# Kernel tuning notes

Measured on AMD Instinct MI355X. Metric: run time of the kernel, lower is better.

## Reference

```python
import jax, jax.numpy as jnp
import numpy as np

EPS = 1e-7  # K.epsilon()

def squash(v, axis=-1):
    sn = jnp.sum(jnp.square(v), axis=axis, keepdims=True)
    scale = sn / (1.0 + sn) / jnp.sqrt(sn + EPS)
    return scale * v

def setup_inputs() -> dict:
    key = jax.random.key(0)
    k1, k2, k3 = jax.random.split(key, 3)
    B, In, Din = 32, 2048, 8
    N, Dout, C = 64, 16, 32
    x = jax.random.normal(k1, (B, In, Din), dtype=jnp.float32)
    W = jax.random.normal(k2, (N, C, Dout, Din), dtype=jnp.float32) * 0.1
    B_bias = jax.random.normal(k3, (N, Dout), dtype=jnp.float32) * 0.1
    return {"x": x, "W": W, "B_bias": B_bias}

def reference(x, W, B_bias):
    routings = 3
    N, C, Dout, Din = W.shape
    In = x.shape[1]
    # repeat channel weights to cover all input capsules: [N, In, Dout, Din]
    W2 = jnp.repeat(W, In // C, axis=1)
    # vote vectors: inputs_hat[b,n,i,d] = sum_k x[b,i,k] * W2[n,i,d,k]
    inputs_hat = jnp.einsum('bik,nidk->bnid', x, W2)  # [B, N, In, Dout]
    b = jnp.zeros(inputs_hat.shape[:3], dtype=inputs_hat.dtype)  # [B, N, In]
    outputs = None
    for i in range(routings):
        c = jax.nn.softmax(b, axis=1)  # softmax over num_capsule axis
        s = jnp.einsum('bni,bnid->bnd', c, inputs_hat) + B_bias
        outputs = squash(s)
        if i < routings - 1:
            b = b + jnp.einsum('bnd,bnid->bni', outputs, inputs_hat)
    return outputs
```

## Files before the change

kernel.cpp:

```cpp
#include <hip/hip_runtime.h>
#include <math.h>

constexpr int B_    = 32;
constexpr int In_   = 2048;
constexpr int Din_  = 8;
constexpr int N_    = 64;
constexpr int Dout_ = 16;
constexpr int C_    = 32;
constexpr int ICP   = 64;
constexpr float EPS = 1e-7f;


__global__ __launch_bounds__(256) void caps_v0(
    const float* __restrict__ x, const float* __restrict__ W,
    const float* __restrict__ bias, float* __restrict__ v0)
{
    const int b = blockIdx.x >> 3, j = blockIdx.x & 7;
    const int t = threadIdx.x;

    __shared__ float xbar[C_][Din_];

    {
        const int c = t >> 3, k = t & 7;
        const float* xp = x + (size_t)b * In_ * Din_ + (size_t)c * ICP * Din_ + k;
        float acc = 0.f;
        #pragma unroll 8
        for (int i = 0; i < ICP; ++i) acc += xp[i * Din_];
        xbar[c][k] = acc * (1.f / 64.f);
    }
    __syncthreads();

    {
        const int nl = t >> 5, lane32 = t & 31;
        const int d = lane32 >> 1, h = lane32 & 1;
        const int n = j * 8 + nl;

        float a = 0.f;
        #pragma unroll
        for (int cc = 0; cc < 16; ++cc) {
            const int c2 = cc * 2 + h;
            const float4* wp = (const float4*)(W + (((size_t)n * C_ + c2) * Dout_ + d) * Din_);
            const float4 w0 = wp[0], w1 = wp[1];
            a += w0.x * xbar[c2][0] + w0.y * xbar[c2][1] + w0.z * xbar[c2][2] + w0.w * xbar[c2][3]
               + w1.x * xbar[c2][4] + w1.y * xbar[c2][5] + w1.z * xbar[c2][6] + w1.w * xbar[c2][7];
        }
        a += __shfl_xor(a, 1);
        a += bias[n * Dout_ + d];

        float sn = a * a;
        sn += __shfl_xor(sn, 2);
        sn += __shfl_xor(sn, 4);
        sn += __shfl_xor(sn, 8);
        sn += __shfl_xor(sn, 16);
        const float sc = sn / (1.f + sn) / sqrtf(sn + EPS);
        if (h == 0) v0[(size_t)b * 1024 + n * Dout_ + d] = a * sc;
    }
}

__global__ __launch_bounds__(256) void caps_route(
    const float* __restrict__ x, const float* __restrict__ W,
    const float* __restrict__ bias, const float* __restrict__ v0buf,
    const float* __restrict__ s_prev, float* __restrict__ s_next)
{
    const int b = blockIdx.x >> 5;
    const int c = blockIdx.x & 31;
    const int t = threadIdx.x;
    const int w = t >> 6, l = t & 63;
    const int n4 = t >> 2, q4 = t & 3;

    __shared__ float Us[N_][8];
    __shared__ float xs[ICP][8];
    __shared__ float lg[ICP][68];
    __shared__ float ps[4][ICP];
    __shared__ float inv_s[ICP];
    __shared__ float ys[4][N_][8];

    float4 vv;
    {
        const size_t vo = (size_t)b * 1024 + n4 * 16 + q4 * 4;
        const float4 v0v = *(const float4*)(v0buf + vo);
        if (s_prev) {
            float4 a = *(const float4*)(s_prev + vo);
            const float4 bb = *(const float4*)(bias + n4 * 16 + q4 * 4);
            a.x += bb.x; a.y += bb.y; a.z += bb.z; a.w += bb.w;
            float sn = a.x * a.x + a.y * a.y + a.z * a.z + a.w * a.w;
            sn += __shfl_xor(sn, 1);
            sn += __shfl_xor(sn, 2);
            const float sc = sn / (1.f + sn) / sqrtf(sn + EPS);
            vv.x = a.x * sc + v0v.x; vv.y = a.y * sc + v0v.y;
            vv.z = a.z * sc + v0v.z; vv.w = a.w * sc + v0v.w;
        } else {
            vv = v0v;
        }
    }

    {
        const float vd[4] = {vv.x, vv.y, vv.z, vv.w};
        float pU[8] = {0, 0, 0, 0, 0, 0, 0, 0};
        #pragma unroll
        for (int dd = 0; dd < 4; ++dd) {
            const int d = q4 * 4 + dd;
            const float4* wp = (const float4*)(W + (((size_t)n4 * 32 + c) * 16 + d) * 8);
            const float4 w0 = wp[0], w1 = wp[1];
            const float v_ = vd[dd];
            pU[0] += v_ * w0.x; pU[1] += v_ * w0.y; pU[2] += v_ * w0.z; pU[3] += v_ * w0.w;
            pU[4] += v_ * w1.x; pU[5] += v_ * w1.y; pU[6] += v_ * w1.z; pU[7] += v_ * w1.w;
        }
        #pragma unroll
        for (int k = 0; k < 8; ++k) {
            pU[k] += __shfl_xor(pU[k], 1);
            pU[k] += __shfl_xor(pU[k], 2);
        }
        float2 u2; u2.x = pU[2 * q4]; u2.y = pU[2 * q4 + 1];
        *(float2*)&Us[n4][2 * q4] = u2;
    }

    float xr[8];
    {
        const float4* xp = (const float4*)(x + ((size_t)b * In_ + c * ICP + l) * 8);
        const float4 x0 = xp[0], x1 = xp[1];
        xr[0] = x0.x; xr[1] = x0.y; xr[2] = x0.z; xr[3] = x0.w;
        xr[4] = x1.x; xr[5] = x1.y; xr[6] = x1.z; xr[7] = x1.w;
        if (w == 0) { *(float4*)&xs[l][0] = x0; *(float4*)&xs[l][4] = x1; }
    }
    __syncthreads();

    {
        float e[16];
        float ssum = 0.f;
        #pragma unroll
        for (int nn = 0; nn < 16; ++nn) {
            const int n = w * 16 + nn;
            const float4 u0 = *(const float4*)&Us[n][0];
            const float4 u1 = *(const float4*)&Us[n][4];
            const float a = u0.x * xr[0] + u0.y * xr[1] + u0.z * xr[2] + u0.w * xr[3]
                          + u1.x * xr[4] + u1.y * xr[5] + u1.z * xr[6] + u1.w * xr[7];
            const float ee = __expf(a);
            e[nn] = ee; ssum += ee;
        }
        #pragma unroll
        for (int qq = 0; qq < 4; ++qq) {
            float4 o;
            o.x = e[qq * 4 + 0]; o.y = e[qq * 4 + 1]; o.z = e[qq * 4 + 2]; o.w = e[qq * 4 + 3];
            *(float4*)&lg[l][w * 16 + qq * 4] = o;
        }
        ps[w][l] = ssum;
    }
    __syncthreads();

    if (t < 64) inv_s[t] = 1.f / (ps[0][t] + ps[1][t] + ps[2][t] + ps[3][t]);
    __syncthreads();

    {
        const int nq = l >> 2, kq = l & 3;
        float y[8] = {0, 0, 0, 0, 0, 0, 0, 0};
        #pragma unroll
        for (int ii = 0; ii < 16; ++ii) {
            const int i = w * 16 + ii;
            const float4 cw = *(const float4*)&lg[i][nq * 4];
            const float iv = inv_s[i];
            const float2 x2 = *(const float2*)&xs[i][kq * 2];
            const float c0 = cw.x * iv, c1 = cw.y * iv, c2 = cw.z * iv, c3 = cw.w * iv;
            y[0] += c0 * x2.x; y[1] += c0 * x2.y;
            y[2] += c1 * x2.x; y[3] += c1 * x2.y;
            y[4] += c2 * x2.x; y[5] += c2 * x2.y;
            y[6] += c3 * x2.x; y[7] += c3 * x2.y;
        }
        #pragma unroll
        for (int jj = 0; jj < 4; ++jj) {
            float2 o; o.x = y[2 * jj]; o.y = y[2 * jj + 1];
            *(float2*)&ys[w][nq * 4 + jj][kq * 2] = o;
        }
    }
    __syncthreads();

    {
        float yn[8];
        #pragma unroll
        for (int k = 0; k < 8; ++k)
            yn[k] = ys[0][n4][k] + ys[1][n4][k] + ys[2][n4][k] + ys[3][n4][k];
        float* sdst = s_next + (size_t)b * 1024 + n4 * 16 + q4 * 4;
        #pragma unroll
        for (int dd = 0; dd < 4; ++dd) {
            const int d = q4 * 4 + dd;
            const float4* wp = (const float4*)(W + (((size_t)n4 * 32 + c) * 16 + d) * 8);
            const float4 w0 = wp[0], w1 = wp[1];
            const float sv = w0.x * yn[0] + w0.y * yn[1] + w0.z * yn[2] + w0.w * yn[3]
                           + w1.x * yn[4] + w1.y * yn[5] + w1.z * yn[6] + w1.w * yn[7];
            atomicAdd(sdst + dd, sv);
        }
    }
}

__global__ __launch_bounds__(256) void caps_out(
    const float* __restrict__ s_src, const float* __restrict__ bias,
    float* __restrict__ out)
{
    const int b = blockIdx.x, t = threadIdx.x;
    const int n = t >> 2, q = t & 3;

    float4 a = *(const float4*)(s_src + (size_t)b * 1024 + n * 16 + q * 4);
    const float4 bb = *(const float4*)(bias + n * 16 + q * 4);
    a.x += bb.x; a.y += bb.y; a.z += bb.z; a.w += bb.w;

    float sn = a.x * a.x + a.y * a.y + a.z * a.z + a.w * a.w;
    sn += __shfl_xor(sn, 1);
    sn += __shfl_xor(sn, 2);
    const float sc = sn / (1.f + sn) / sqrtf(sn + EPS);
    float4 o;
    o.x = a.x * sc; o.y = a.y * sc; o.z = a.z * sc; o.w = a.w * sc;
    *(float4*)(out + (size_t)b * 1024 + t * 4) = o;
}

extern "C" void kernel_launch(void* const* d_in, const int* in_sizes, int n_in,
                              void* d_out, int out_size, void* d_ws, size_t ws_size,
                              hipStream_t stream) {
    const float* x    = (const float*)d_in[0];
    const float* W    = (const float*)d_in[1];
    const float* bias = (const float*)d_in[2];
    float* out = (float*)d_out;

    float* ws = (float*)d_ws;
    float* v0 = ws;
    float* s1 = v0 + (size_t)B_ * N_ * Dout_;
    float* s2 = s1 + (size_t)B_ * N_ * Dout_;

    caps_v0   <<<256,  256, 0, stream>>>(x, W, bias, v0);
    caps_route<<<1024, 256, 0, stream>>>(x, W, bias, v0, nullptr, s1);
    caps_route<<<1024, 256, 0, stream>>>(x, W, bias, v0, s1,      s2);
    caps_out  <<<32,   256, 0, stream>>>(s2, bias, out);
}
```

Measured before the change: 102.5 us.

## Replace atomic accumulation of routing sums with per-channel partial buffers

Each routing block now writes its per-channel contribution to a dedicated partial buffer slot instead of issuing atomicAdds into a shared per-batch accumulator. The consumers (the next routing pass and the output kernel) sum the 32 channel partials themselves before the squash. This removes atomic contention, since 32 blocks previously hit the same addresses, and removes any reliance on a zeroed workspace. The cost is that every block of the second routing pass re-reads 32 partials per element from a 4 MB buffer, which adds a lot of redundant L2 traffic.

```diff
diff --git a/kernel.cpp b/kernel.cpp
--- a/kernel.cpp
+++ b/kernel.cpp
@@ -60,7 +60,7 @@
 __global__ __launch_bounds__(256) void caps_route(
     const float* __restrict__ x, const float* __restrict__ W,
     const float* __restrict__ bias, const float* __restrict__ v0buf,
-    const float* __restrict__ s_prev, float* __restrict__ s_next)
+    const float* __restrict__ sp_prev, float* __restrict__ sp_out)
 {
     const int b = blockIdx.x >> 5;
     const int c = blockIdx.x & 31;
@@ -79,10 +79,13 @@
     {
         const size_t vo = (size_t)b * 1024 + n4 * 16 + q4 * 4;
         const float4 v0v = *(const float4*)(v0buf + vo);
-        if (s_prev) {
-            float4 a = *(const float4*)(s_prev + vo);
-            const float4 bb = *(const float4*)(bias + n4 * 16 + q4 * 4);
-            a.x += bb.x; a.y += bb.y; a.z += bb.z; a.w += bb.w;
+        if (sp_prev) {
+            float4 a = *(const float4*)(bias + n4 * 16 + q4 * 4);
+            #pragma unroll 8
+            for (int cc = 0; cc < 32; ++cc) {
+                const float4 p = *(const float4*)(sp_prev + (((size_t)b * 32 + cc) * 64 + n4) * 16 + q4 * 4);
+                a.x += p.x; a.y += p.y; a.z += p.z; a.w += p.w;
+            }
             float sn = a.x * a.x + a.y * a.y + a.z * a.z + a.w * a.w;
             sn += __shfl_xor(sn, 1);
             sn += __shfl_xor(sn, 2);
@@ -179,30 +182,32 @@
         #pragma unroll
         for (int k = 0; k < 8; ++k)
             yn[k] = ys[0][n4][k] + ys[1][n4][k] + ys[2][n4][k] + ys[3][n4][k];
-        float* sdst = s_next + (size_t)b * 1024 + n4 * 16 + q4 * 4;
+        float4 o; float* op = (float*)&o;
         #pragma unroll
         for (int dd = 0; dd < 4; ++dd) {
             const int d = q4 * 4 + dd;
             const float4* wp = (const float4*)(W + (((size_t)n4 * 32 + c) * 16 + d) * 8);
             const float4 w0 = wp[0], w1 = wp[1];
-            const float sv = w0.x * yn[0] + w0.y * yn[1] + w0.z * yn[2] + w0.w * yn[3]
-                           + w1.x * yn[4] + w1.y * yn[5] + w1.z * yn[6] + w1.w * yn[7];
-            atomicAdd(sdst + dd, sv);
-        }
+            op[dd] = w0.x * yn[0] + w0.y * yn[1] + w0.z * yn[2] + w0.w * yn[3]
+                   + w1.x * yn[4] + w1.y * yn[5] + w1.z * yn[6] + w1.w * yn[7];
+        }
+        *(float4*)(sp_out + (((size_t)b * 32 + c) * 64 + n4) * 16 + q4 * 4) = o;
     }
 }
 
 __global__ __launch_bounds__(256) void caps_out(
-    const float* __restrict__ s_src, const float* __restrict__ bias,
+    const float* __restrict__ sp_src, const float* __restrict__ bias,
     float* __restrict__ out)
 {
     const int b = blockIdx.x, t = threadIdx.x;
-    const int n = t >> 2, q = t & 3;
-
-    float4 a = *(const float4*)(s_src + (size_t)b * 1024 + n * 16 + q * 4);
-    const float4 bb = *(const float4*)(bias + n * 16 + q * 4);
-    a.x += bb.x; a.y += bb.y; a.z += bb.z; a.w += bb.w;
-
+    const int n4 = t >> 2, q4 = t & 3;
+
+    float4 a = *(const float4*)(bias + n4 * 16 + q4 * 4);
+    #pragma unroll 8
+    for (int cc = 0; cc < 32; ++cc) {
+        const float4 p = *(const float4*)(sp_src + (((size_t)b * 32 + cc) * 64 + n4) * 16 + q4 * 4);
+        a.x += p.x; a.y += p.y; a.z += p.z; a.w += p.w;
+    }
     float sn = a.x * a.x + a.y * a.y + a.z * a.z + a.w * a.w;
     sn += __shfl_xor(sn, 1);
     sn += __shfl_xor(sn, 2);
@@ -220,13 +225,13 @@
     const float* bias = (const float*)d_in[2];
     float* out = (float*)d_out;
 
-    float* ws = (float*)d_ws;
-    float* v0 = ws;
-    float* s1 = v0 + (size_t)B_ * N_ * Dout_;
-    float* s2 = s1 + (size_t)B_ * N_ * Dout_;
+    float* ws  = (float*)d_ws;
+    float* sp1 = ws;
+    float* sp2 = sp1 + (size_t)B_ * C_ * N_ * Dout_;
+    float* v0  = sp2 + (size_t)B_ * C_ * N_ * Dout_;
 
     caps_v0   <<<256,  256, 0, stream>>>(x, W, bias, v0);
-    caps_route<<<1024, 256, 0, stream>>>(x, W, bias, v0, nullptr, s1);
-    caps_route<<<1024, 256, 0, stream>>>(x, W, bias, v0, s1,      s2);
-    caps_out  <<<32,   256, 0, stream>>>(s2, bias, out);
-}
+    caps_route<<<1024, 256, 0, stream>>>(x, W, bias, v0, nullptr, sp1);
+    caps_route<<<1024, 256, 0, stream>>>(x, W, bias, v0, sp1,     sp2);
+    caps_out  <<<32,   256, 0, stream>>>(sp2, bias, out);
+}
```

Result: faster. 96.63 us (-5.7%).
